# Performance work log

Measured on AMD Instinct MI355X. Metric: run time of the kernel, lower is better.

## Reference

```python
import jax, jax.numpy as jnp
import numpy as np

B, R, S = 1, 8192, 128          # batch, rays, samples per ray
GRID = 128                      # occupancy grid resolution per axis
AMIN, AMAX = -1.5, 1.5          # scene AABB
STEP = (AMAX - AMIN) * float(np.sqrt(3.0)) / S   # render_step_size (aabb diagonal / S)
H = 64                          # MLP width
LX, LD = 4, 2                   # posenc levels for xyz / viewdirs


def posenc(x, L):
    freqs = 2.0 ** jnp.arange(L, dtype=x.dtype)            # [L]
    ang = x[..., None] * freqs                             # [...,3,L]
    enc = jnp.concatenate([jnp.sin(ang), jnp.cos(ang)], axis=-1)
    return jnp.concatenate([x, enc.reshape(x.shape[:-1] + (-1,))], axis=-1)


def setup_inputs() -> dict:
    key = jax.random.key(0)
    ks = jax.random.split(key, 12)
    def w(k, i, o):
        return jax.random.normal(k, (i, o), jnp.float32) / np.sqrt(float(i))
    rays_o = jax.random.uniform(ks[0], (B, R, 3), jnp.float32, -1.0, 1.0)
    vd = jax.random.normal(ks[1], (B, R, 3), jnp.float32)
    viewdirs = vd / jnp.linalg.norm(vd, axis=-1, keepdims=True)
    occ_grid = jax.random.uniform(ks[2], (GRID, GRID, GRID)) > 0.4
    in_x = 3 + 3 * 2 * LX   # 27
    in_d = 3 + 3 * 2 * LD   # 15
    return {
        "rays_o": rays_o, "viewdirs": viewdirs, "occ_grid": occ_grid,
        "W1": w(ks[3], in_x, H), "b1": jnp.zeros((H,), jnp.float32),
        "W2": w(ks[4], H, H), "b2": jnp.zeros((H,), jnp.float32),
        "Ws": w(ks[5], H, 1), "bs": jnp.zeros((1,), jnp.float32),
        "Wc": w(ks[6], H, H), "Wd": w(ks[7], in_d, H), "bc": jnp.zeros((H,), jnp.float32),
        "Wr": w(ks[8], H, 3), "br": jnp.zeros((3,), jnp.float32),
    }


def reference(rays_o, viewdirs, occ_grid, W1, b1, W2, b2, Ws, bs, Wc, Wd, bc, Wr, br):
    o = rays_o.reshape(-1, 3)
    d = viewdirs.reshape(-1, 3)
    # ray / AABB intersection -> per-ray marching segment [t_near, t_far)
    safe_d = jnp.where(jnp.abs(d) < 1e-8, 1e-8, d)
    t1 = (AMIN - o) / safe_d
    t2 = (AMAX - o) / safe_d
    t_near = jnp.maximum(jnp.max(jnp.minimum(t1, t2), axis=-1), 0.0)   # [NR]
    t_far = jnp.min(jnp.maximum(t1, t2), axis=-1)                      # [NR]
    # fixed-count uniform marching; invalid samples masked to sigma=0
    t = t_near[:, None] + (jnp.arange(S, dtype=jnp.float32) + 0.5) * STEP  # [NR,S]
    in_seg = t < t_far[:, None]
    pts = o[:, None, :] + d[:, None, :] * t[..., None]                 # [NR,S,3]
    # occupancy grid gather (irregular access hot path)
    cell = (pts - AMIN) / (AMAX - AMIN) * GRID
    idx = jnp.clip(jnp.floor(cell).astype(jnp.int32), 0, GRID - 1)
    in_box = jnp.all((cell >= 0) & (cell < GRID), axis=-1)
    occ = occ_grid[idx[..., 0], idx[..., 1], idx[..., 2]]
    valid = in_seg & in_box & occ                                      # [NR,S]
    # NeRF MLP: density from encoded position, color from feature + encoded dir
    pe_x = posenc(pts, LX)                       # [NR,S,27]
    pe_d = posenc(d, LD)                         # [NR,15]
    h = jax.nn.relu(pe_x @ W1 + b1)
    h = jax.nn.relu(h @ W2 + b2)                 # [NR,S,H]
    sigma = jax.nn.relu((h @ Ws + bs)[..., 0]) * valid   # [NR,S]
    g = jax.nn.relu(h @ Wc + (pe_d @ Wd)[:, None, :] + bc)
    rgb = jax.nn.sigmoid(g @ Wr + br)            # [NR,S,3]
    # alpha compositing (nerfacc.rendering equivalent)
    sdelta = sigma * STEP
    alpha = 1.0 - jnp.exp(-sdelta)
    T = jnp.exp(-(jnp.cumsum(sdelta, axis=-1) - sdelta))   # exclusive transmittance
    w = T * alpha                                # [NR,S]
    rgb_map = jnp.sum(w[..., None] * rgb, axis=1)          # [NR,3]
    acc = jnp.sum(w, axis=1)                               # [NR]
    depth = jnp.sum(w * t, axis=1)                         # [NR]
    rgb_map = rgb_map + (1.0 - acc)[:, None]               # white background
    return (rgb_map.reshape(B, R, 3), depth.reshape(B, R, 1), acc.reshape(B, R, 1))
```

## Files before the change

kernel.cpp:

```cpp
#include <hip/hip_runtime.h>
#include <math.h>


typedef _Float16 f16x8 __attribute__((ext_vector_type(8)));
typedef _Float16 f16x4 __attribute__((ext_vector_type(4)));
typedef float f32x4 __attribute__((ext_vector_type(4)));

static constexpr float STEPf = 0.040594940802395566f;

static __device__ __forceinline__ unsigned pk2(float a, float b) {
    return __builtin_bit_cast(unsigned, __builtin_amdgcn_cvt_pkrtz(a, b));
}
static __device__ __forceinline__ f16x8 mk8(unsigned a, unsigned b, unsigned c, unsigned d) {
    uint4 u = make_uint4(a, b, c, d);
    return __builtin_bit_cast(f16x8, u);
}
static __device__ __forceinline__ f16x4 pkh(const f32x4 c) {
    uint2 u;
    u.x = pk2(fmaxf(c[0], 0.f), fmaxf(c[1], 0.f));
    u.y = pk2(fmaxf(c[2], 0.f), fmaxf(c[3], 0.f));
    return __builtin_bit_cast(f16x4, u);
}
static __device__ __forceinline__ float rfl(float x) {
    return __builtin_bit_cast(float, __builtin_amdgcn_readfirstlane(__builtin_bit_cast(int, x)));
}

extern "C" __global__ void __launch_bounds__(256, 8)
nerf_mfma(const float* __restrict__ rays_o, const float* __restrict__ viewdirs,
          const void* __restrict__ occ,
          const float* __restrict__ W1g, const float* __restrict__ b1g,
          const float* __restrict__ W2g, const float* __restrict__ b2g,
          const float* __restrict__ Wsg, const float* __restrict__ bsg,
          const float* __restrict__ Wcg, const float* __restrict__ Wdg,
          const float* __restrict__ bcg, const float* __restrict__ Wrg,
          const float* __restrict__ brg,
          float* __restrict__ out, int nrays)
{
    __shared__ __align__(16) unsigned char sW1[64 * 64];
    __shared__ __align__(16) unsigned char sW2[64 * 128];
    __shared__ __align__(16) unsigned char sWc[64 * 128];
    __shared__ __align__(16) unsigned char sHC[16 * 128];
    __shared__ __align__(16) float sWs[64];
    __shared__ __align__(16) float sB1[64], sB2[64];
    __shared__ __align__(16) float sPdB[4][64];
    __shared__ int sKind;

    const int tid = threadIdx.x;

    for (int idx = tid; idx < 1024; idx += 256)
        ((uint32_t*)sW1)[idx] = 0u;
    __syncthreads();
    for (int idx = tid; idx < 27 * 64; idx += 256) {
        const int k = idx >> 6, h = idx & 63;
        *(_Float16*)(sW1 + h * 64 + (((k >> 3) ^ (h & 3)) << 4) + ((k & 7) << 1)) =
            (_Float16)W1g[idx];
    }
    for (int idx = tid; idx < 64 * 64; idx += 256) {
        const int k = idx >> 6, h = idx & 63;
        const int off = h * 128 + ((((k >> 2) ^ ((h & 7) << 1)) << 3)) + ((k & 3) << 1);
        *(_Float16*)(sW2 + off) = (_Float16)W2g[idx];
        *(_Float16*)(sWc + off) = (_Float16)Wcg[idx];
    }
    for (int idx = tid; idx < 192; idx += 256) {
        const int kk = idx / 3, c = idx - 3 * kk;
        const _Float16 v = (_Float16)Wrg[idx];
        #pragma unroll
        for (int r = 0; r < 16; ++r) {
            if ((r % 3) == c) {
                const int off = r * 128 + ((((kk >> 2) ^ ((r & 7) << 1)) << 3)) + ((kk & 3) << 1);
                *(_Float16*)(sHC + off) = v;
            }
        }
    }
    if (tid < 64) {
        sB1[tid] = b1g[tid]; sB2[tid] = b2g[tid];
        sWs[tid] = Wsg[tid];
    }
    if (tid == 0) {
        const int*   oi = (const int*)occ;
        const float* of = (const float*)occ;
        bool i32ok = true, f32ok = true;
        for (int k = 0; k < 64; ++k) {
            if (oi[k] != 0 && oi[k] != 1) i32ok = false;
            const float f = of[k];
            if (!(f == 0.f || f == 1.f)) f32ok = false;
        }
        sKind = (i32ok || f32ok) ? 1 : 0;
    }
    __syncthreads();

    const int lane = tid & 63;
    const int wid  = tid >> 6;
    const int kind = sKind;
    const int lh = lane & 15, g = lane >> 4;
    const int swz8 = (lh & 7) << 1;

    const float bsV = bsg[0];
    const float br0 = brg[0], br1 = brg[1], br2 = brg[2];

    const int ray = __builtin_amdgcn_readfirstlane((int)(blockIdx.x << 2) + wid);
    if (ray >= nrays) return;

    const float ox = rays_o[ray * 3 + 0], oy = rays_o[ray * 3 + 1], oz = rays_o[ray * 3 + 2];
    const float dxv = viewdirs[ray * 3 + 0], dyv = viewdirs[ray * 3 + 1], dzv = viewdirs[ray * 3 + 2];
    float t_near, t_far;
    {
        const float sdx = fabsf(dxv) < 1e-8f ? 1e-8f : dxv;
        const float sdy = fabsf(dyv) < 1e-8f ? 1e-8f : dyv;
        const float sdz = fabsf(dzv) < 1e-8f ? 1e-8f : dzv;
        const float t1x = (-1.5f - ox) / sdx, t2x = (1.5f - ox) / sdx;
        const float t1y = (-1.5f - oy) / sdy, t2y = (1.5f - oy) / sdy;
        const float t1z = (-1.5f - oz) / sdz, t2z = (1.5f - oz) / sdz;
        t_near = rfl(fmaxf(fmaxf(fminf(t1x, t2x), fminf(t1y, t2y)),
                           fmaxf(fminf(t1z, t2z), 0.f)));
        t_far  = rfl(fminf(fminf(fmaxf(t1x, t2x), fmaxf(t1y, t2y)), fmaxf(t1z, t2z)));
    }

    float W = 0.f, WT = 0.f, Rr = 0.f, Gg = 0.f, Bb = 0.f;

    if (t_near < t_far) {
        {
            float ped[15];
            ped[0] = dxv; ped[1] = dyv; ped[2] = dzv;
            const float dc[3] = {dxv, dyv, dzv};
            #pragma unroll
            for (int c = 0; c < 3; ++c) {
                float s1, c1;
                __sincosf(dc[c], &s1, &c1);
                ped[3 + c * 4 + 0] = s1;
                ped[3 + c * 4 + 1] = 2.f * s1 * c1;
                ped[3 + c * 4 + 2] = c1;
                ped[3 + c * 4 + 3] = 1.f - 2.f * s1 * s1;
            }
            float pd = 0.f;
            #pragma unroll
            for (int i = 0; i < 15; ++i) pd += ped[i] * Wdg[i * 64 + lane];
            sPdB[wid][lane] = pd + bcg[lane];
        }

        float f = 1.f;
        #pragma unroll 1
        for (int bt = 0; bt < 8; ++bt) {
            const float tS = t_near + ((float)((bt << 4) | lh) + 0.5f) * STEPf;
            const bool in_seg = tS < t_far;
            if (__ballot(in_seg) == 0ULL) break;

            bool valid;
            {
                const float px = ox + dxv * tS, py = oy + dyv * tS, pz = oz + dzv * tS;
                const float cx = (px + 1.5f) * (128.f / 3.f);
                const float cy = (py + 1.5f) * (128.f / 3.f);
                const float cz = (pz + 1.5f) * (128.f / 3.f);
                const bool in_box = (cx >= 0.f) & (cx < 128.f) & (cy >= 0.f) & (cy < 128.f)
                                  & (cz >= 0.f) & (cz < 128.f);
                const int ix = min(max((int)floorf(cx), 0), 127);
                const int iy = min(max((int)floorf(cy), 0), 127);
                const int iz = min(max((int)floorf(cz), 0), 127);
                const int ci = (ix << 14) | (iy << 7) | iz;
                const unsigned raw = (kind == 0) ? (unsigned)((const unsigned char*)occ)[ci]
                                                 : ((const unsigned*)occ)[ci];
                valid = in_seg & in_box & (raw != 0u);
            }
            if (__ballot(valid) == 0ULL) continue;

            f16x8 bx;
            {
                const float qx = ox + dxv * tS, qy = oy + dyv * tS, qz = oz + dzv * tS;
                const float u = (g < 2) ? qx : ((g == 2) ? qy : qz);
                const float v = (g == 1) ? qy : ((g == 2) ? qz : 0.f);
                float su1, cu1, sv1, cv1;
                __sincosf(u, &su1, &cu1);
                __sincosf(v, &sv1, &cv1);
                const float su2 = 2.f * su1 * cu1, cu2 = 1.f - 2.f * su1 * su1;
                const float su4 = 2.f * su2 * cu2, cu4 = 1.f - 2.f * su2 * su2;
                const float su8 = 2.f * su4 * cu4, cu8 = 1.f - 2.f * su4 * su4;
                const float sv2 = 2.f * sv1 * cv1, cv2 = 1.f - 2.f * sv1 * sv1;
                const float sv4 = 2.f * sv2 * cv2, cv4 = 1.f - 2.f * sv2 * sv2;
                const float sv8 = 2.f * sv4 * cv4;
                const bool g0 = (g == 0);
                const float f0 = g0 ? qx : cu2;
                const float f1 = g0 ? qy : cu4;
                const float f2 = g0 ? qz : cu8;
                const float f3 = g0 ? su1 : sv1;
                const float f4 = g0 ? su2 : sv2;
                const float f5 = g0 ? su4 : sv4;
                const float f6 = g0 ? su8 : sv8;
                const float f7 = g0 ? cu1 : ((g == 3) ? 0.f : cv1);
                bx = mk8(pk2(f0, f1), pk2(f2, f3), pk2(f4, f5), pk2(f6, f7));
            }

            f16x4 bh1[4];
            #pragma unroll
            for (int mt = 0; mt < 4; ++mt) {
                const f32x4 bf = *(const f32x4*)&sB1[16 * mt + 4 * g];
                const f16x8 a = *(const f16x8*)(sW1 + (16 * mt + lh) * 64 + ((g ^ (lh & 3)) << 4));
                f32x4 c = __builtin_amdgcn_mfma_f32_16x16x32_f16(a, bx, bf, 0, 0, 0);
                bh1[mt] = pkh(c);
            }
            f16x4 bh2[4];
            float sp = 0.f;
            #pragma unroll
            for (int mt = 0; mt < 4; ++mt) {
                const int row = (16 * mt + lh) * 128;
                const f16x4 a0 = *(const f16x4*)(sW2 + row + (((0 + g) ^ swz8) << 3));
                const f16x4 a1 = *(const f16x4*)(sW2 + row + (((4 + g) ^ swz8) << 3));
                const f16x4 a2 = *(const f16x4*)(sW2 + row + (((8 + g) ^ swz8) << 3));
                const f16x4 a3 = *(const f16x4*)(sW2 + row + (((12 + g) ^ swz8) << 3));
                const f32x4 bf = *(const f32x4*)&sB2[16 * mt + 4 * g];
                const f32x4 ws = *(const f32x4*)&sWs[16 * mt + 4 * g];
                f32x4 c = __builtin_amdgcn_mfma_f32_16x16x16f16(a0, bh1[0], bf, 0, 0, 0);
                c = __builtin_amdgcn_mfma_f32_16x16x16f16(a1, bh1[1], c, 0, 0, 0);
                c = __builtin_amdgcn_mfma_f32_16x16x16f16(a2, bh1[2], c, 0, 0, 0);
                c = __builtin_amdgcn_mfma_f32_16x16x16f16(a3, bh1[3], c, 0, 0, 0);
                const float r0 = fmaxf(c[0], 0.f), r1 = fmaxf(c[1], 0.f);
                const float r2 = fmaxf(c[2], 0.f), r3 = fmaxf(c[3], 0.f);
                sp += ws[0] * r0 + ws[1] * r1 + ws[2] * r2 + ws[3] * r3;
                uint2 u; u.x = pk2(r0, r1); u.y = pk2(r2, r3);
                bh2[mt] = __builtin_bit_cast(f16x4, u);
            }
            f32x4 accC;
            #pragma unroll
            for (int mt = 0; mt < 4; ++mt) {
                const int row = (16 * mt + lh) * 128;
                const f16x4 a0 = *(const f16x4*)(sWc + row + (((0 + g) ^ swz8) << 3));
                const f16x4 a1 = *(const f16x4*)(sWc + row + (((4 + g) ^ swz8) << 3));
                const f16x4 a2 = *(const f16x4*)(sWc + row + (((8 + g) ^ swz8) << 3));
                const f16x4 a3 = *(const f16x4*)(sWc + row + (((12 + g) ^ swz8) << 3));
                const f32x4 pdf = *(const f32x4*)&sPdB[wid][16 * mt + 4 * g];
                const f16x4 aC = *(const f16x4*)(sHC + lh * 128 + (((4 * mt + g) ^ swz8) << 3));
                f32x4 c = __builtin_amdgcn_mfma_f32_16x16x16f16(a0, bh2[0], pdf, 0, 0, 0);
                c = __builtin_amdgcn_mfma_f32_16x16x16f16(a1, bh2[1], c, 0, 0, 0);
                c = __builtin_amdgcn_mfma_f32_16x16x16f16(a2, bh2[2], c, 0, 0, 0);
                c = __builtin_amdgcn_mfma_f32_16x16x16f16(a3, bh2[3], c, 0, 0, 0);
                const f16x4 bgf = pkh(c);
                f32x4 ca = (mt == 0) ? f32x4{0.f, 0.f, 0.f, 0.f} : accC;
                accC = __builtin_amdgcn_mfma_f32_16x16x16f16(aC, bgf, ca, 0, 0, 0);
            }
            sp += __shfl_xor(sp, 16);
            sp += __shfl_xor(sp, 32);
            const float crS = (g == 1) ? accC[2] : (g == 2) ? accC[1] : accC[0];
            const float cgS = (g == 0) ? accC[1] : (g == 1) ? accC[0]
                            : (g == 2) ? accC[2] : accC[1];
            const float cbS = (g == 0) ? accC[2] : (g == 1) ? accC[1]
                            : (g == 2) ? accC[0] : accC[2];

            const float sigma = valid ? fmaxf(sp + bsV, 0.f) : 0.f;
            const float rC = 1.f / (1.f + __expf(-(crS + br0)));
            const float gC = 1.f / (1.f + __expf(-(cgS + br1)));
            const float bC = 1.f / (1.f + __expf(-(cbS + br2)));

            const float sdelta = sigma * STEPf;
            float scan = sdelta;
            #pragma unroll
            for (int off = 1; off < 16; off <<= 1) {
                const float n = __shfl_up(scan, off);
                if (lh >= off) scan += n;
            }
            const float T     = __expf(-(scan - sdelta));
            const float alpha = 1.f - __expf(-sdelta);
            const float w = f * T * alpha;
            W  += w;
            WT += w * tS;
            Rr += w * rC;
            Gg += w * gC;
            Bb += w * bC;
            const float Stile = rfl(__shfl(scan, (lane & 48) | 15));
            f *= __expf(-Stile);
            if (f < 6e-6f) break;
        }
    }

    #pragma unroll
    for (int off = 1; off < 16; off <<= 1) {
        W  += __shfl_xor(W,  off);
        WT += __shfl_xor(WT, off);
        Rr += __shfl_xor(Rr, off);
        Gg += __shfl_xor(Gg, off);
        Bb += __shfl_xor(Bb, off);
    }
    if (lane == 0) {
        const float bg_ = 1.f - W;
        out[ray * 3 + 0] = Rr + bg_;
        out[ray * 3 + 1] = Gg + bg_;
        out[ray * 3 + 2] = Bb + bg_;
        out[3 * nrays + ray] = WT;
        out[4 * nrays + ray] = W;
    }
}

extern "C" void kernel_launch(void* const* d_in, const int* in_sizes, int n_in,
                              void* d_out, int out_size, void* d_ws, size_t ws_size,
                              hipStream_t stream) {
    const float* rays_o   = (const float*)d_in[0];
    const float* viewdirs = (const float*)d_in[1];
    const void*  occ      = (const void*) d_in[2];
    const float* W1 = (const float*)d_in[3];
    const float* b1 = (const float*)d_in[4];
    const float* W2 = (const float*)d_in[5];
    const float* b2 = (const float*)d_in[6];
    const float* Ws = (const float*)d_in[7];
    const float* bs = (const float*)d_in[8];
    const float* Wc = (const float*)d_in[9];
    const float* Wd = (const float*)d_in[10];
    const float* bc = (const float*)d_in[11];
    const float* Wr = (const float*)d_in[12];
    const float* br = (const float*)d_in[13];
    float* out = (float*)d_out;

    const int nrays = in_sizes[0] / 3;
    const int nblocks = (nrays + 3) / 4;

    nerf_mfma<<<nblocks, 256, 0, stream>>>(rays_o, viewdirs, occ,
                                           W1, b1, W2, b2, Ws, bs, Wc, Wd, bc, Wr, br,
                                           out, nrays);
}
```

Measured before the change: 44.04 us.

## Process two sample tiles per march iteration to interleave independent MFMA chains

The ray-march loop now handles two 16-sample tiles (A and B) per iteration, interleaving their MFMA chains so that independent matrix ops can hide each other's latency. It also shares the weight loads from LDS across both tiles. The launch-bounds occupancy hint of 8 is dropped so the doubled live state can use more registers. In exchange, early termination is coarser: tile B is computed even when A already saturated or B is empty, which wastes work. Lower occupancy may reduce latency hiding across waves.

New measurement: 49.67 us. +12.8%, slower.

```diff
diff --git a/kernel.cpp b/kernel.cpp
--- a/kernel.cpp
+++ b/kernel.cpp
@@ -25,7 +25,7 @@
     return __builtin_bit_cast(float, __builtin_amdgcn_readfirstlane(__builtin_bit_cast(int, x)));
 }
 
-extern "C" __global__ void __launch_bounds__(256, 8)
+extern "C" __global__ void __launch_bounds__(256)
 nerf_mfma(const float* __restrict__ rays_o, const float* __restrict__ viewdirs,
           const void* __restrict__ occ,
           const float* __restrict__ W1g, const float* __restrict__ b1g,
@@ -138,134 +138,175 @@
             sPdB[wid][lane] = pd + bcg[lane];
         }
 
+        auto validAt = [&](float t, bool inseg) -> bool {
+            const float px = ox + dxv * t, py = oy + dyv * t, pz = oz + dzv * t;
+            const float cx = (px + 1.5f) * (128.f / 3.f);
+            const float cy = (py + 1.5f) * (128.f / 3.f);
+            const float cz = (pz + 1.5f) * (128.f / 3.f);
+            const bool in_box = (cx >= 0.f) & (cx < 128.f) & (cy >= 0.f) & (cy < 128.f)
+                              & (cz >= 0.f) & (cz < 128.f);
+            const int ix = min(max((int)floorf(cx), 0), 127);
+            const int iy = min(max((int)floorf(cy), 0), 127);
+            const int iz = min(max((int)floorf(cz), 0), 127);
+            const int ci = (ix << 14) | (iy << 7) | iz;
+            const unsigned raw = (kind == 0) ? (unsigned)((const unsigned char*)occ)[ci]
+                                             : ((const unsigned*)occ)[ci];
+            return inseg & in_box & (raw != 0u);
+        };
+        auto posenc = [&](float t) -> f16x8 {
+            const float qx = ox + dxv * t, qy = oy + dyv * t, qz = oz + dzv * t;
+            const float u = (g < 2) ? qx : ((g == 2) ? qy : qz);
+            const float v = (g == 1) ? qy : ((g == 2) ? qz : 0.f);
+            float su1, cu1, sv1, cv1;
+            __sincosf(u, &su1, &cu1);
+            __sincosf(v, &sv1, &cv1);
+            const float su2 = 2.f * su1 * cu1, cu2 = 1.f - 2.f * su1 * su1;
+            const float su4 = 2.f * su2 * cu2, cu4 = 1.f - 2.f * su2 * su2;
+            const float su8 = 2.f * su4 * cu4, cu8 = 1.f - 2.f * su4 * su4;
+            const float sv2 = 2.f * sv1 * cv1, cv2 = 1.f - 2.f * sv1 * sv1;
+            const float sv4 = 2.f * sv2 * cv2, cv4 = 1.f - 2.f * sv2 * sv2;
+            const float sv8 = 2.f * sv4 * cv4;
+            const bool g0 = (g == 0);
+            const float f0 = g0 ? qx : cu2;
+            const float f1 = g0 ? qy : cu4;
+            const float f2 = g0 ? qz : cu8;
+            const float f3 = g0 ? su1 : sv1;
+            const float f4 = g0 ? su2 : sv2;
+            const float f5 = g0 ? su4 : sv4;
+            const float f6 = g0 ? su8 : sv8;
+            const float f7 = g0 ? cu1 : ((g == 3) ? 0.f : cv1);
+            return mk8(pk2(f0, f1), pk2(f2, f3), pk2(f4, f5), pk2(f6, f7));
+        };
+
         float f = 1.f;
         #pragma unroll 1
-        for (int bt = 0; bt < 8; ++bt) {
-            const float tS = t_near + ((float)((bt << 4) | lh) + 0.5f) * STEPf;
-            const bool in_seg = tS < t_far;
-            if (__ballot(in_seg) == 0ULL) break;
-
-            bool valid;
-            {
-                const float px = ox + dxv * tS, py = oy + dyv * tS, pz = oz + dzv * tS;
-                const float cx = (px + 1.5f) * (128.f / 3.f);
-                const float cy = (py + 1.5f) * (128.f / 3.f);
-                const float cz = (pz + 1.5f) * (128.f / 3.f);
-                const bool in_box = (cx >= 0.f) & (cx < 128.f) & (cy >= 0.f) & (cy < 128.f)
-                                  & (cz >= 0.f) & (cz < 128.f);
-                const int ix = min(max((int)floorf(cx), 0), 127);
-                const int iy = min(max((int)floorf(cy), 0), 127);
-                const int iz = min(max((int)floorf(cz), 0), 127);
-                const int ci = (ix << 14) | (iy << 7) | iz;
-                const unsigned raw = (kind == 0) ? (unsigned)((const unsigned char*)occ)[ci]
-                                                 : ((const unsigned*)occ)[ci];
-                valid = in_seg & in_box & (raw != 0u);
+        for (int bp = 0; bp < 4; ++bp) {
+            const float tA = t_near + ((float)((bp << 5) | lh) + 0.5f) * STEPf;
+            const float tB = tA + 16.f * STEPf;
+            const bool insegA = tA < t_far;
+            const bool insegB = tB < t_far;
+            if (__ballot(insegA) == 0ULL) break;
+
+            const bool validA = validAt(tA, insegA);
+            const bool validB = validAt(tB, insegB);
+
+            if (__ballot(validA | validB) != 0ULL) {
+                const f16x8 bxA = posenc(tA);
+                const f16x8 bxB = posenc(tB);
+
+                f16x4 bh1A[4], bh1B[4];
+                #pragma unroll
+                for (int mt = 0; mt < 4; ++mt) {
+                    const f32x4 bf = *(const f32x4*)&sB1[16 * mt + 4 * g];
+                    const f16x8 a = *(const f16x8*)(sW1 + (16 * mt + lh) * 64 + ((g ^ (lh & 3)) << 4));
+                    f32x4 cA = __builtin_amdgcn_mfma_f32_16x16x32_f16(a, bxA, bf, 0, 0, 0);
+                    f32x4 cB = __builtin_amdgcn_mfma_f32_16x16x32_f16(a, bxB, bf, 0, 0, 0);
+                    bh1A[mt] = pkh(cA);
+                    bh1B[mt] = pkh(cB);
+                }
+                f16x4 bh2A[4], bh2B[4];
+                float spA = 0.f, spB = 0.f;
+                #pragma unroll
+                for (int mt = 0; mt < 4; ++mt) {
+                    const int row = (16 * mt + lh) * 128;
+                    const f16x4 a0 = *(const f16x4*)(sW2 + row + (((0 + g) ^ swz8) << 3));
+                    const f16x4 a1 = *(const f16x4*)(sW2 + row + (((4 + g) ^ swz8) << 3));
+                    const f16x4 a2 = *(const f16x4*)(sW2 + row + (((8 + g) ^ swz8) << 3));
+                    const f16x4 a3 = *(const f16x4*)(sW2 + row + (((12 + g) ^ swz8) << 3));
+                    const f32x4 bf = *(const f32x4*)&sB2[16 * mt + 4 * g];
+                    const f32x4 ws = *(const f32x4*)&sWs[16 * mt + 4 * g];
+                    f32x4 cA = __builtin_amdgcn_mfma_f32_16x16x16f16(a0, bh1A[0], bf, 0, 0, 0);
+                    f32x4 cB = __builtin_amdgcn_mfma_f32_16x16x16f16(a0, bh1B[0], bf, 0, 0, 0);
+                    cA = __builtin_amdgcn_mfma_f32_16x16x16f16(a1, bh1A[1], cA, 0, 0, 0);
+                    cB = __builtin_amdgcn_mfma_f32_16x16x16f16(a1, bh1B[1], cB, 0, 0, 0);
+                    cA = __builtin_amdgcn_mfma_f32_16x16x16f16(a2, bh1A[2], cA, 0, 0, 0);
+                    cB = __builtin_amdgcn_mfma_f32_16x16x16f16(a2, bh1B[2], cB, 0, 0, 0);
+                    cA = __builtin_amdgcn_mfma_f32_16x16x16f16(a3, bh1A[3], cA, 0, 0, 0);
+                    cB = __builtin_amdgcn_mfma_f32_16x16x16f16(a3, bh1B[3], cB, 0, 0, 0);
+                    const float rA0 = fmaxf(cA[0], 0.f), rA1 = fmaxf(cA[1], 0.f);
+                    const float rA2 = fmaxf(cA[2], 0.f), rA3 = fmaxf(cA[3], 0.f);
+                    const float rB0 = fmaxf(cB[0], 0.f), rB1 = fmaxf(cB[1], 0.f);
+                    const float rB2 = fmaxf(cB[2], 0.f), rB3 = fmaxf(cB[3], 0.f);
+                    spA += ws[0] * rA0 + ws[1] * rA1 + ws[2] * rA2 + ws[3] * rA3;
+                    spB += ws[0] * rB0 + ws[1] * rB1 + ws[2] * rB2 + ws[3] * rB3;
+                    uint2 uA; uA.x = pk2(rA0, rA1); uA.y = pk2(rA2, rA3);
+                    uint2 uB; uB.x = pk2(rB0, rB1); uB.y = pk2(rB2, rB3);
+                    bh2A[mt] = __builtin_bit_cast(f16x4, uA);
+                    bh2B[mt] = __builtin_bit_cast(f16x4, uB);
+                }
+                f32x4 accCA, accCB;
+                #pragma unroll
+                for (int mt = 0; mt < 4; ++mt) {
+                    const int row = (16 * mt + lh) * 128;
+                    const f16x4 a0 = *(const f16x4*)(sWc + row + (((0 + g) ^ swz8) << 3));
+                    const f16x4 a1 = *(const f16x4*)(sWc + row + (((4 + g) ^ swz8) << 3));
+                    const f16x4 a2 = *(const f16x4*)(sWc + row + (((8 + g) ^ swz8) << 3));
+                    const f16x4 a3 = *(const f16x4*)(sWc + row + (((12 + g) ^ swz8) << 3));
+                    const f32x4 pdf = *(const f32x4*)&sPdB[wid][16 * mt + 4 * g];
+                    const f16x4 aC = *(const f16x4*)(sHC + lh * 128 + (((4 * mt + g) ^ swz8) << 3));
+                    f32x4 cA = __builtin_amdgcn_mfma_f32_16x16x16f16(a0, bh2A[0], pdf, 0, 0, 0);
+                    f32x4 cB = __builtin_amdgcn_mfma_f32_16x16x16f16(a0, bh2B[0], pdf, 0, 0, 0);
+                    cA = __builtin_amdgcn_mfma_f32_16x16x16f16(a1, bh2A[1], cA, 0, 0, 0);
+                    cB = __builtin_amdgcn_mfma_f32_16x16x16f16(a1, bh2B[1], cB, 0, 0, 0);
+                    cA = __builtin_amdgcn_mfma_f32_16x16x16f16(a2, bh2A[2], cA, 0, 0, 0);
+                    cB = __builtin_amdgcn_mfma_f32_16x16x16f16(a2, bh2B[2], cB, 0, 0, 0);
+                    cA = __builtin_amdgcn_mfma_f32_16x16x16f16(a3, bh2A[3], cA, 0, 0, 0);
+                    cB = __builtin_amdgcn_mfma_f32_16x16x16f16(a3, bh2B[3], cB, 0, 0, 0);
+                    const f16x4 bgfA = pkh(cA);
+                    const f16x4 bgfB = pkh(cB);
+                    f32x4 caA = (mt == 0) ? f32x4{0.f, 0.f, 0.f, 0.f} : accCA;
+                    f32x4 caB = (mt == 0) ? f32x4{0.f, 0.f, 0.f, 0.f} : accCB;
+                    accCA = __builtin_amdgcn_mfma_f32_16x16x16f16(aC, bgfA, caA, 0, 0, 0);
+                    accCB = __builtin_amdgcn_mfma_f32_16x16x16f16(aC, bgfB, caB, 0, 0, 0);
+                }
+                spA += __shfl_xor(spA, 16);  spA += __shfl_xor(spA, 32);
+                spB += __shfl_xor(spB, 16);  spB += __shfl_xor(spB, 32);
+                const float crA = (g == 1) ? accCA[2] : (g == 2) ? accCA[1] : accCA[0];
+                const float cgA = (g == 0) ? accCA[1] : (g == 1) ? accCA[0]
+                                : (g == 2) ? accCA[2] : accCA[1];
+                const float cbA = (g == 0) ? accCA[2] : (g == 1) ? accCA[1]
+                                : (g == 2) ? accCA[0] : accCA[2];
+                const float crB = (g == 1) ? accCB[2] : (g == 2) ? accCB[1] : accCB[0];
+                const float cgB = (g == 0) ? accCB[1] : (g == 1) ? accCB[0]
+                                : (g == 2) ? accCB[2] : accCB[1];
+                const float cbB = (g == 0) ? accCB[2] : (g == 1) ? accCB[1]
+                                : (g == 2) ? accCB[0] : accCB[2];
+
+                const float sigmaA = validA ? fmaxf(spA + bsV, 0.f) : 0.f;
+                const float sigmaB = validB ? fmaxf(spB + bsV, 0.f) : 0.f;
+                const float rCA = 1.f / (1.f + __expf(-(crA + br0)));
+                const float gCA = 1.f / (1.f + __expf(-(cgA + br1)));
+                const float bCA = 1.f / (1.f + __expf(-(cbA + br2)));
+                const float rCB = 1.f / (1.f + __expf(-(crB + br0)));
+                const float gCB = 1.f / (1.f + __expf(-(cgB + br1)));
+                const float bCB = 1.f / (1.f + __expf(-(cbB + br2)));
+
+                const float sdA = sigmaA * STEPf;
+                const float sdB = sigmaB * STEPf;
+                float scA = sdA, scB = sdB;
+                #pragma unroll
+                for (int off = 1; off < 16; off <<= 1) {
+                    const float nA = __shfl_up(scA, off);
+                    const float nB = __shfl_up(scB, off);
+                    if (lh >= off) { scA += nA; scB += nB; }
+                }
+                {
+                    const float T = __expf(-(scA - sdA));
+                    const float alpha = 1.f - __expf(-sdA);
+                    const float w = f * T * alpha;
+                    W += w; WT += w * tA; Rr += w * rCA; Gg += w * gCA; Bb += w * bCA;
+                    f *= __expf(-rfl(__shfl(scA, (lane & 48) | 15)));
+                }
+                {
+                    const float T = __expf(-(scB - sdB));
+                    const float alpha = 1.f - __expf(-sdB);
+                    const float w = f * T * alpha;
+                    W += w; WT += w * tB; Rr += w * rCB; Gg += w * gCB; Bb += w * bCB;
+                    f *= __expf(-rfl(__shfl(scB, (lane & 48) | 15)));
+                }
             }
-            if (__ballot(valid) == 0ULL) continue;
-
-            f16x8 bx;
-            {
-                const float qx = ox + dxv * tS, qy = oy + dyv * tS, qz = oz + dzv * tS;
-                const float u = (g < 2) ? qx : ((g == 2) ? qy : qz);
-                const float v = (g == 1) ? qy : ((g == 2) ? qz : 0.f);
-                float su1, cu1, sv1, cv1;
-                __sincosf(u, &su1, &cu1);
-                __sincosf(v, &sv1, &cv1);
-                const float su2 = 2.f * su1 * cu1, cu2 = 1.f - 2.f * su1 * su1;
-                const float su4 = 2.f * su2 * cu2, cu4 = 1.f - 2.f * su2 * su2;
-                const float su8 = 2.f * su4 * cu4, cu8 = 1.f - 2.f * su4 * su4;
-                const float sv2 = 2.f * sv1 * cv1, cv2 = 1.f - 2.f * sv1 * sv1;
-                const float sv4 = 2.f * sv2 * cv2, cv4 = 1.f - 2.f * sv2 * sv2;
-                const float sv8 = 2.f * sv4 * cv4;
-                const bool g0 = (g == 0);
-                const float f0 = g0 ? qx : cu2;
-                const float f1 = g0 ? qy : cu4;
-                const float f2 = g0 ? qz : cu8;
-                const float f3 = g0 ? su1 : sv1;
-                const float f4 = g0 ? su2 : sv2;
-                const float f5 = g0 ? su4 : sv4;
-                const float f6 = g0 ? su8 : sv8;
-                const float f7 = g0 ? cu1 : ((g == 3) ? 0.f : cv1);
-                bx = mk8(pk2(f0, f1), pk2(f2, f3), pk2(f4, f5), pk2(f6, f7));
-            }
-
-            f16x4 bh1[4];
-            #pragma unroll
-            for (int mt = 0; mt < 4; ++mt) {
-                const f32x4 bf = *(const f32x4*)&sB1[16 * mt + 4 * g];
-                const f16x8 a = *(const f16x8*)(sW1 + (16 * mt + lh) * 64 + ((g ^ (lh & 3)) << 4));
-                f32x4 c = __builtin_amdgcn_mfma_f32_16x16x32_f16(a, bx, bf, 0, 0, 0);
-                bh1[mt] = pkh(c);
-            }
-            f16x4 bh2[4];
-            float sp = 0.f;
-            #pragma unroll
-            for (int mt = 0; mt < 4; ++mt) {
-                const int row = (16 * mt + lh) * 128;
-                const f16x4 a0 = *(const f16x4*)(sW2 + row + (((0 + g) ^ swz8) << 3));
-                const f16x4 a1 = *(const f16x4*)(sW2 + row + (((4 + g) ^ swz8) << 3));
-                const f16x4 a2 = *(const f16x4*)(sW2 + row + (((8 + g) ^ swz8) << 3));
-                const f16x4 a3 = *(const f16x4*)(sW2 + row + (((12 + g) ^ swz8) << 3));
-                const f32x4 bf = *(const f32x4*)&sB2[16 * mt + 4 * g];
-                const f32x4 ws = *(const f32x4*)&sWs[16 * mt + 4 * g];
-                f32x4 c = __builtin_amdgcn_mfma_f32_16x16x16f16(a0, bh1[0], bf, 0, 0, 0);
-                c = __builtin_amdgcn_mfma_f32_16x16x16f16(a1, bh1[1], c, 0, 0, 0);
-                c = __builtin_amdgcn_mfma_f32_16x16x16f16(a2, bh1[2], c, 0, 0, 0);
-                c = __builtin_amdgcn_mfma_f32_16x16x16f16(a3, bh1[3], c, 0, 0, 0);
-                const float r0 = fmaxf(c[0], 0.f), r1 = fmaxf(c[1], 0.f);
-                const float r2 = fmaxf(c[2], 0.f), r3 = fmaxf(c[3], 0.f);
-                sp += ws[0] * r0 + ws[1] * r1 + ws[2] * r2 + ws[3] * r3;
-                uint2 u; u.x = pk2(r0, r1); u.y = pk2(r2, r3);
-                bh2[mt] = __builtin_bit_cast(f16x4, u);
-            }
-            f32x4 accC;
-            #pragma unroll
-            for (int mt = 0; mt < 4; ++mt) {
-                const int row = (16 * mt + lh) * 128;
-                const f16x4 a0 = *(const f16x4*)(sWc + row + (((0 + g) ^ swz8) << 3));
-                const f16x4 a1 = *(const f16x4*)(sWc + row + (((4 + g) ^ swz8) << 3));
-                const f16x4 a2 = *(const f16x4*)(sWc + row + (((8 + g) ^ swz8) << 3));
-                const f16x4 a3 = *(const f16x4*)(sWc + row + (((12 + g) ^ swz8) << 3));
-                const f32x4 pdf = *(const f32x4*)&sPdB[wid][16 * mt + 4 * g];
-                const f16x4 aC = *(const f16x4*)(sHC + lh * 128 + (((4 * mt + g) ^ swz8) << 3));
-                f32x4 c = __builtin_amdgcn_mfma_f32_16x16x16f16(a0, bh2[0], pdf, 0, 0, 0);
-                c = __builtin_amdgcn_mfma_f32_16x16x16f16(a1, bh2[1], c, 0, 0, 0);
-                c = __builtin_amdgcn_mfma_f32_16x16x16f16(a2, bh2[2], c, 0, 0, 0);
-                c = __builtin_amdgcn_mfma_f32_16x16x16f16(a3, bh2[3], c, 0, 0, 0);
-                const f16x4 bgf = pkh(c);
-                f32x4 ca = (mt == 0) ? f32x4{0.f, 0.f, 0.f, 0.f} : accC;
-                accC = __builtin_amdgcn_mfma_f32_16x16x16f16(aC, bgf, ca, 0, 0, 0);
-            }
-            sp += __shfl_xor(sp, 16);
-            sp += __shfl_xor(sp, 32);
-            const float crS = (g == 1) ? accC[2] : (g == 2) ? accC[1] : accC[0];
-            const float cgS = (g == 0) ? accC[1] : (g == 1) ? accC[0]
-                            : (g == 2) ? accC[2] : accC[1];
-            const float cbS = (g == 0) ? accC[2] : (g == 1) ? accC[1]
-                            : (g == 2) ? accC[0] : accC[2];
-
-            const float sigma = valid ? fmaxf(sp + bsV, 0.f) : 0.f;
-            const float rC = 1.f / (1.f + __expf(-(crS + br0)));
-            const float gC = 1.f / (1.f + __expf(-(cgS + br1)));
-            const float bC = 1.f / (1.f + __expf(-(cbS + br2)));
-
-            const float sdelta = sigma * STEPf;
-            float scan = sdelta;
-            #pragma unroll
-            for (int off = 1; off < 16; off <<= 1) {
-                const float n = __shfl_up(scan, off);
-                if (lh >= off) scan += n;
-            }
-            const float T     = __expf(-(scan - sdelta));
-            const float alpha = 1.f - __expf(-sdelta);
-            const float w = f * T * alpha;
-            W  += w;
-            WT += w * tS;
-            Rr += w * rC;
-            Gg += w * gC;
-            Bb += w * bC;
-            const float Stile = rfl(__shfl(scan, (lane & 48) | 15));
-            f *= __expf(-Stile);
+
+            if (__ballot(insegB) == 0ULL) break;
             if (f < 6e-6f) break;
         }
     }
```
